# Performance work log

Hardware: AMD Instinct MI355X
Metric: run time of the kernel (lower is better)

## Reference

```python
import jax, jax.numpy as jnp
import numpy as np

OUTPUT_SIZE = 512
MEMORY_SIZE = 64
N_HALF = 131072          # terrain / population vision length each
N_EDGES = 16777216       # enabled connections
NUM_INPUT_NODES = 2 * N_HALF + MEMORY_SIZE * OUTPUT_SIZE + 1  # +1 bias


def setup_inputs() -> dict:
    key = jax.random.key(0)
    k = jax.random.split(key, 5)
    return {
        "terrain": jax.random.normal(k[0], (N_HALF,), dtype=jnp.float32),
        "population": jax.random.normal(k[1], (N_HALF,), dtype=jnp.float32),
        "memory": jnp.zeros((MEMORY_SIZE, OUTPUT_SIZE), dtype=jnp.float32),
        "src": jax.random.randint(k[2], (N_EDGES,), 0, NUM_INPUT_NODES),
        "dst": jax.random.randint(k[3], (N_EDGES,), 0, OUTPUT_SIZE),
        "w": jax.random.normal(k[4], (N_EDGES,), dtype=jnp.float32),
    }


def reference(terrain, population, memory, src, dst, w):
    # Build the flat input-node activation vector exactly like forward():
    # [terrain, population, memory.flatten(), bias=1]
    x = jnp.concatenate([
        terrain,
        population,
        memory.reshape(-1),
        jnp.ones((1,), dtype=terrain.dtype),
    ])  # [NUM_INPUT_NODES]
    # Per-edge weighted gather, then scatter-add into output nodes.
    # Output nodes use identity activation (only hidden nodes get ReLU,
    # and the minimal-init topology has input->output edges only).
    contrib = x[src] * w                                   # [N_EDGES]
    out = jax.ops.segment_sum(contrib, dst, num_segments=OUTPUT_SIZE)
    return out[None, :]  # [1, OUTPUT_SIZE], matching torch.stack(..., dim=1)
```

## Files before the change

kernel.cpp:

```cpp
#include <hip/hip_runtime.h>

#define N_HALF   131072
#define MEM_ELEMS (64 * 512)
#define NIN      (2 * N_HALF + MEM_ELEMS + 1)
#define NEDGES   16777216
#define NOUT     512
#define TPB      256
#define NBLK1    2048
#define GROUPS_PER_BLOCK (NEDGES / NBLK1 / 4)
#define ITERS    (GROUPS_PER_BLOCK / TPB)

__global__ __launch_bounds__(TPB) void build_x_kernel(
    const float* __restrict__ terrain,
    const float* __restrict__ pop,
    const float* __restrict__ mem,
    float* __restrict__ x)
{
    int i = blockIdx.x * TPB + threadIdx.x;
    if (i >= NIN) return;
    float v;
    if (i < N_HALF)            v = terrain[i];
    else if (i < 2 * N_HALF)   v = pop[i - N_HALF];
    else if (i < NIN - 1)      v = mem[i - 2 * N_HALF];
    else                       v = 1.0f;
    x[i] = v;
}

__device__ __forceinline__ float fetch_direct(int s,
    const float* __restrict__ terrain,
    const float* __restrict__ pop,
    const float* __restrict__ mem)
{
    if (s < 2 * N_HALF)
        return (s < N_HALF) ? terrain[s] : pop[s - N_HALF];
    return (s < NIN - 1) ? mem[s - 2 * N_HALF] : 1.0f;
}

__global__ __launch_bounds__(TPB) void zero_out_kernel(float* __restrict__ out)
{
    int i = blockIdx.x * TPB + threadIdx.x;
    if (i < NOUT) out[i] = 0.0f;
}

template <int MODE>
__global__ __launch_bounds__(TPB) void edge_kernel(
    const int4*   __restrict__ src4,
    const int4*   __restrict__ dst4,
    const float4* __restrict__ w4,
    const float*  __restrict__ x,
    const float*  __restrict__ terrain,
    const float*  __restrict__ pop,
    const float*  __restrict__ mem,
    float* __restrict__ outp)
{
    __shared__ float acc[NOUT];
    const int t = threadIdx.x;
    acc[t] = 0.0f;
    acc[t + TPB] = 0.0f;
    __syncthreads();

    const int base = blockIdx.x * GROUPS_PER_BLOCK + t;
#pragma unroll
    for (int j = 0; j < ITERS; ++j) {
        const int g = base + j * TPB;
        const int4   s = src4[g];
        const int4   d = dst4[g];
        const float4 w = w4[g];
        float vx, vy, vz, vw;
        if (MODE == 2) {
            vx = fetch_direct(s.x, terrain, pop, mem);
            vy = fetch_direct(s.y, terrain, pop, mem);
            vz = fetch_direct(s.z, terrain, pop, mem);
            vw = fetch_direct(s.w, terrain, pop, mem);
        } else {
            vx = x[s.x];
            vy = x[s.y];
            vz = x[s.z];
            vw = x[s.w];
        }
        unsafeAtomicAdd(&acc[d.x], vx * w.x);
        unsafeAtomicAdd(&acc[d.y], vy * w.y);
        unsafeAtomicAdd(&acc[d.z], vz * w.z);
        unsafeAtomicAdd(&acc[d.w], vw * w.w);
    }
    __syncthreads();

    if (MODE == 0) {
        outp[(size_t)blockIdx.x * NOUT + t]       = acc[t];
        outp[(size_t)blockIdx.x * NOUT + t + TPB] = acc[t + TPB];
    } else {
        unsafeAtomicAdd(&outp[t],       acc[t]);
        unsafeAtomicAdd(&outp[t + TPB], acc[t + TPB]);
    }
}

__global__ __launch_bounds__(TPB) void reduce_kernel(
    const float* __restrict__ partials, float* __restrict__ out)
{
    const float4* __restrict__ p4 = (const float4*)partials;
    const int t = threadIdx.x;
    float4 s = make_float4(0.f, 0.f, 0.f, 0.f);
    for (int k = t; k < NBLK1; k += TPB) {
        float4 v = p4[(size_t)k * (NOUT / 4) + blockIdx.x];
        s.x += v.x; s.y += v.y; s.z += v.z; s.w += v.w;
    }
#pragma unroll
    for (int off = 32; off; off >>= 1) {
        s.x += __shfl_down(s.x, off, 64);
        s.y += __shfl_down(s.y, off, 64);
        s.z += __shfl_down(s.z, off, 64);
        s.w += __shfl_down(s.w, off, 64);
    }
    __shared__ float l[4][4];
    const int wid = t >> 6, lane = t & 63;
    if (lane == 0) {
        l[wid][0] = s.x; l[wid][1] = s.y; l[wid][2] = s.z; l[wid][3] = s.w;
    }
    __syncthreads();
    if (t < 4) {
        out[blockIdx.x * 4 + t] = l[0][t] + l[1][t] + l[2][t] + l[3][t];
    }
}

extern "C" void kernel_launch(void* const* d_in, const int* in_sizes, int n_in,
                              void* d_out, int out_size, void* d_ws, size_t ws_size,
                              hipStream_t stream)
{
    const float* terrain = (const float*)d_in[0];
    const float* pop     = (const float*)d_in[1];
    const float* mem     = (const float*)d_in[2];
    const int*   src     = (const int*)d_in[3];
    const int*   dst     = (const int*)d_in[4];
    const float* w       = (const float*)d_in[5];
    float* out = (float*)d_out;

    const size_t X_BYTES  = (size_t)NIN * 4;
    const size_t PART_OFF = 1179904;
    const size_t NEED     = PART_OFF + (size_t)NBLK1 * NOUT * 4;

    float* x        = (float*)d_ws;
    float* partials = (float*)((char*)d_ws + PART_OFF);

    if (ws_size >= NEED) {
        build_x_kernel<<<(NIN + TPB - 1) / TPB, TPB, 0, stream>>>(terrain, pop, mem, x);
        edge_kernel<0><<<NBLK1, TPB, 0, stream>>>(
            (const int4*)src, (const int4*)dst, (const float4*)w,
            x, terrain, pop, mem, partials);
        reduce_kernel<<<NOUT / 4, TPB, 0, stream>>>(partials, out);
    } else if (ws_size >= X_BYTES) {
        build_x_kernel<<<(NIN + TPB - 1) / TPB, TPB, 0, stream>>>(terrain, pop, mem, x);
        zero_out_kernel<<<(NOUT + TPB - 1) / TPB, TPB, 0, stream>>>(out);
        edge_kernel<1><<<NBLK1, TPB, 0, stream>>>(
            (const int4*)src, (const int4*)dst, (const float4*)w,
            x, terrain, pop, mem, out);
    } else {
        zero_out_kernel<<<(NOUT + TPB - 1) / TPB, TPB, 0, stream>>>(out);
        edge_kernel<2><<<NBLK1, TPB, 0, stream>>>(
            (const int4*)src, (const int4*)dst, (const float4*)w,
            nullptr, terrain, pop, mem, out);
    }
}
```

Baseline: 274.0 us.

## Software-pipeline edge loads with nontemporal prefetch and restructure partial reduction

The edge kernel now loads src/dst/weight vectors for the next batch of four groups using nontemporal loads while gathering and accumulating the current batch. This is meant to hide global memory latency on the streaming edge arrays and keep them from polluting cache, at the cost of more registers. The final reduction switches to row-block partial sums combined with global atomics, and the output zeroing is folded into build_x. The atomic reduction makes the summation order nondeterministic.

```diff
diff --git a/kernel.cpp b/kernel.cpp
--- a/kernel.cpp
+++ b/kernel.cpp
@@ -9,14 +9,24 @@
 #define NBLK1    2048
 #define GROUPS_PER_BLOCK (NEDGES / NBLK1 / 4)
 #define ITERS    (GROUPS_PER_BLOCK / TPB)
+#define BATCH    4
+#define NBATCH   (ITERS / BATCH)
+
+#define RBLK          128
+#define ROWS_PER_BLK  (NBLK1 / RBLK)
+
+typedef int   vint4   __attribute__((ext_vector_type(4)));
+typedef float vfloat4 __attribute__((ext_vector_type(4)));
 
 __global__ __launch_bounds__(TPB) void build_x_kernel(
     const float* __restrict__ terrain,
     const float* __restrict__ pop,
     const float* __restrict__ mem,
-    float* __restrict__ x)
+    float* __restrict__ x,
+    float* __restrict__ out)
 {
     int i = blockIdx.x * TPB + threadIdx.x;
+    if (i < NOUT) out[i] = 0.0f;
     if (i >= NIN) return;
     float v;
     if (i < N_HALF)            v = terrain[i];
@@ -44,13 +54,13 @@
 
 template <int MODE>
 __global__ __launch_bounds__(TPB) void edge_kernel(
-    const int4*   __restrict__ src4,
-    const int4*   __restrict__ dst4,
-    const float4* __restrict__ w4,
-    const float*  __restrict__ x,
-    const float*  __restrict__ terrain,
-    const float*  __restrict__ pop,
-    const float*  __restrict__ mem,
+    const vint4*   __restrict__ src4,
+    const vint4*   __restrict__ dst4,
+    const vfloat4* __restrict__ w4,
+    const float*   __restrict__ x,
+    const float*   __restrict__ terrain,
+    const float*   __restrict__ pop,
+    const float*   __restrict__ mem,
     float* __restrict__ outp)
 {
     __shared__ float acc[NOUT];
@@ -60,28 +70,66 @@
     __syncthreads();
 
     const int base = blockIdx.x * GROUPS_PER_BLOCK + t;
+
+    vint4   s[BATCH], d[BATCH];
+    vfloat4 wv[BATCH];
 #pragma unroll
-    for (int j = 0; j < ITERS; ++j) {
-        const int g = base + j * TPB;
-        const int4   s = src4[g];
-        const int4   d = dst4[g];
-        const float4 w = w4[g];
-        float vx, vy, vz, vw;
-        if (MODE == 2) {
-            vx = fetch_direct(s.x, terrain, pop, mem);
-            vy = fetch_direct(s.y, terrain, pop, mem);
-            vz = fetch_direct(s.z, terrain, pop, mem);
-            vw = fetch_direct(s.w, terrain, pop, mem);
-        } else {
-            vx = x[s.x];
-            vy = x[s.y];
-            vz = x[s.z];
-            vw = x[s.w];
+    for (int u = 0; u < BATCH; ++u)
+        s[u] = __builtin_nontemporal_load(&src4[base + u * TPB]);
+#pragma unroll
+    for (int u = 0; u < BATCH; ++u)
+        d[u] = __builtin_nontemporal_load(&dst4[base + u * TPB]);
+#pragma unroll
+    for (int u = 0; u < BATCH; ++u)
+        wv[u] = __builtin_nontemporal_load(&w4[base + u * TPB]);
+
+#pragma unroll
+    for (int b = 0; b < NBATCH; ++b) {
+        float g[BATCH][4];
+#pragma unroll
+        for (int u = 0; u < BATCH; ++u) {
+            if (MODE == 2) {
+                g[u][0] = fetch_direct(s[u].x, terrain, pop, mem);
+                g[u][1] = fetch_direct(s[u].y, terrain, pop, mem);
+                g[u][2] = fetch_direct(s[u].z, terrain, pop, mem);
+                g[u][3] = fetch_direct(s[u].w, terrain, pop, mem);
+            } else {
+                g[u][0] = x[s[u].x];
+                g[u][1] = x[s[u].y];
+                g[u][2] = x[s[u].z];
+                g[u][3] = x[s[u].w];
+            }
         }
-        unsafeAtomicAdd(&acc[d.x], vx * w.x);
-        unsafeAtomicAdd(&acc[d.y], vy * w.y);
-        unsafeAtomicAdd(&acc[d.z], vz * w.z);
-        unsafeAtomicAdd(&acc[d.w], vw * w.w);
+
+        vint4   s2[BATCH], d2[BATCH];
+        vfloat4 w2[BATCH];
+        if (b + 1 < NBATCH) {
+            const int nb = base + (b + 1) * BATCH * TPB;
+#pragma unroll
+            for (int u = 0; u < BATCH; ++u)
+                s2[u] = __builtin_nontemporal_load(&src4[nb + u * TPB]);
+#pragma unroll
+            for (int u = 0; u < BATCH; ++u)
+                d2[u] = __builtin_nontemporal_load(&dst4[nb + u * TPB]);
+#pragma unroll
+            for (int u = 0; u < BATCH; ++u)
+                w2[u] = __builtin_nontemporal_load(&w4[nb + u * TPB]);
+        }
+
+#pragma unroll
+        for (int u = 0; u < BATCH; ++u) {
+            unsafeAtomicAdd(&acc[d[u].x], g[u][0] * wv[u].x);
+            unsafeAtomicAdd(&acc[d[u].y], g[u][1] * wv[u].y);
+            unsafeAtomicAdd(&acc[d[u].z], g[u][2] * wv[u].z);
+            unsafeAtomicAdd(&acc[d[u].w], g[u][3] * wv[u].w);
+        }
+
+        if (b + 1 < NBATCH) {
+#pragma unroll
+            for (int u = 0; u < BATCH; ++u) {
+                s[u] = s2[u]; d[u] = d2[u]; wv[u] = w2[u];
+            }
+        }
     }
     __syncthreads();
 
@@ -94,32 +142,22 @@
     }
 }
 
-__global__ __launch_bounds__(TPB) void reduce_kernel(
+__global__ __launch_bounds__(128) void reduce_kernel(
     const float* __restrict__ partials, float* __restrict__ out)
 {
-    const float4* __restrict__ p4 = (const float4*)partials;
-    const int t = threadIdx.x;
-    float4 s = make_float4(0.f, 0.f, 0.f, 0.f);
-    for (int k = t; k < NBLK1; k += TPB) {
-        float4 v = p4[(size_t)k * (NOUT / 4) + blockIdx.x];
-        s.x += v.x; s.y += v.y; s.z += v.z; s.w += v.w;
+    const vfloat4* __restrict__ p4 = (const vfloat4*)partials;
+    const int t  = threadIdx.x;
+    const int r0 = blockIdx.x * ROWS_PER_BLK;
+    vfloat4 s = {0.f, 0.f, 0.f, 0.f};
+#pragma unroll
+    for (int r = 0; r < ROWS_PER_BLK; ++r) {
+        vfloat4 v = p4[(size_t)(r0 + r) * (NOUT / 4) + t];
+        s += v;
     }
-#pragma unroll
-    for (int off = 32; off; off >>= 1) {
-        s.x += __shfl_down(s.x, off, 64);
-        s.y += __shfl_down(s.y, off, 64);
-        s.z += __shfl_down(s.z, off, 64);
-        s.w += __shfl_down(s.w, off, 64);
-    }
-    __shared__ float l[4][4];
-    const int wid = t >> 6, lane = t & 63;
-    if (lane == 0) {
-        l[wid][0] = s.x; l[wid][1] = s.y; l[wid][2] = s.z; l[wid][3] = s.w;
-    }
-    __syncthreads();
-    if (t < 4) {
-        out[blockIdx.x * 4 + t] = l[0][t] + l[1][t] + l[2][t] + l[3][t];
-    }
+    unsafeAtomicAdd(&out[t * 4 + 0], s.x);
+    unsafeAtomicAdd(&out[t * 4 + 1], s.y);
+    unsafeAtomicAdd(&out[t * 4 + 2], s.z);
+    unsafeAtomicAdd(&out[t * 4 + 3], s.w);
 }
 
 extern "C" void kernel_launch(void* const* d_in, const int* in_sizes, int n_in,
@@ -142,21 +180,20 @@
     float* partials = (float*)((char*)d_ws + PART_OFF);
 
     if (ws_size >= NEED) {
-        build_x_kernel<<<(NIN + TPB - 1) / TPB, TPB, 0, stream>>>(terrain, pop, mem, x);
+        build_x_kernel<<<(NIN + TPB - 1) / TPB, TPB, 0, stream>>>(terrain, pop, mem, x, out);
         edge_kernel<0><<<NBLK1, TPB, 0, stream>>>(
-            (const int4*)src, (const int4*)dst, (const float4*)w,
+            (const vint4*)src, (const vint4*)dst, (const vfloat4*)w,
             x, terrain, pop, mem, partials);
-        reduce_kernel<<<NOUT / 4, TPB, 0, stream>>>(partials, out);
+        reduce_kernel<<<RBLK, 128, 0, stream>>>(partials, out);
     } else if (ws_size >= X_BYTES) {
-        build_x_kernel<<<(NIN + TPB - 1) / TPB, TPB, 0, stream>>>(terrain, pop, mem, x);
-        zero_out_kernel<<<(NOUT + TPB - 1) / TPB, TPB, 0, stream>>>(out);
+        build_x_kernel<<<(NIN + TPB - 1) / TPB, TPB, 0, stream>>>(terrain, pop, mem, x, out);
         edge_kernel<1><<<NBLK1, TPB, 0, stream>>>(
-            (const int4*)src, (const int4*)dst, (const float4*)w,
+            (const vint4*)src, (const vint4*)dst, (const vfloat4*)w,
             x, terrain, pop, mem, out);
     } else {
         zero_out_kernel<<<(NOUT + TPB - 1) / TPB, TPB, 0, stream>>>(out);
         edge_kernel<2><<<NBLK1, TPB, 0, stream>>>(
-            (const int4*)src, (const int4*)dst, (const float4*)w,
+            (const vint4*)src, (const vint4*)dst, (const vfloat4*)w,
             nullptr, terrain, pop, mem, out);
     }
 }
```

Measured after the change: 266.9 us. -2.6%, faster.
